# Kernel tuning notes

Hardware: AMD Instinct MI355X
Metric: run time of the kernel (lower is better)

The kernel has to match this reference:

```python
import jax, jax.numpy as jnp
import numpy as np

B, N, S, P, D = 128, 4096, 32, 64, 128  # batch, wafers, stages, PMs, embed dim
NORM = 300.0


def gather(src, idx):
    # src: [B, n, D], idx: [B, m] int -> [B, m, D]
    return jnp.take_along_axis(src, idx[:, :, None], axis=1)


def setup_inputs() -> dict:
    key = jax.random.key(0)
    ks = jax.random.split(key, 16)
    return {
        "encoded_row": jax.random.normal(ks[0], (B, N, D), jnp.float32),
        "encoded_col": jax.random.normal(ks[1], (B, S, D), jnp.float32),
        "clock": jax.random.uniform(ks[2], (B, 1), jnp.float32) * NORM,
        "loc_process_end_time": jax.random.uniform(ks[3], (B, P), jnp.float32) * (2.0 * NORM),
        "W_dyn": jax.random.normal(ks[4], (2, D), jnp.float32) * 0.05,
        "W_concat": jax.random.normal(ks[5], (3 * D, D), jnp.float32) * 0.05,
        "W_robot": jax.random.normal(ks[6], (3 * D, D), jnp.float32) * 0.05,
        "loc_hold_wafer": jax.random.randint(ks[7], (B, P), 0, N),
        "loc_stage": jax.random.randint(ks[8], (B, P), 1, S + 1),
        "robot_arm1_loc": jax.random.randint(ks[9], (B, 1), 0, P + 2),
        "robot_arm2_loc": jax.random.randint(ks[10], (B, 1), 0, P + 2),
        "arm1_recipe": jax.random.randint(ks[11], (B, 1), 0, N),
        "arm2_recipe": jax.random.randint(ks[12], (B, 1), 0, N),
        "arm1_next_stage": jax.random.randint(ks[13], (B, 1), 0, S + 2),
        "arm2_next_stage": jax.random.randint(ks[14], (B, 1), 0, S + 2),
    }


def reference(encoded_row, encoded_col, clock, loc_process_end_time,
              W_dyn, W_concat, W_robot,
              loc_hold_wafer, loc_stage, robot_arm1_loc, robot_arm2_loc,
              arm1_recipe, arm2_recipe, arm1_next_stage, arm2_next_stage):
    dt = encoded_row.dtype
    # ---- get_PM_embedding ----
    clk = jnp.broadcast_to(clock, (B, P))
    remain_prs = jnp.where(loc_process_end_time > clk,
                           loc_process_end_time - clk, 0.0) / NORM
    remain_purge = jnp.zeros_like(remain_prs)
    pm_dyn = jnp.stack([remain_prs, remain_purge], axis=-1) @ W_dyn  # [B,P,D]

    rows_dummy = jnp.concatenate(
        [encoded_row, jnp.zeros((B, 1, D), dt)], axis=1)          # [B,N+1,D]
    lot_idx = jnp.where(loc_hold_wafer >= 0, loc_hold_wafer, N)
    pm_wafer = gather(rows_dummy, lot_idx)                         # [B,P,D]
    pm_stage = gather(encoded_col, loc_stage - 1)                  # [B,P,D]
    pm_emb = jnp.concatenate([pm_stage, pm_wafer, pm_dyn], -1) @ W_concat

    # ---- get_robot_embedding ----
    loc_emb = jnp.concatenate(
        [jnp.zeros((B, 1, D), dt), pm_emb, jnp.ones((B, 1, D), dt)], axis=1)
    cols_pad = jnp.concatenate(
        [jnp.zeros((B, 1, D), dt), encoded_col, jnp.zeros((B, 1, D), dt)], axis=1)

    def arm_embed(loc_idx, recipe, next_stage):
        a_loc = gather(loc_emb, loc_idx)                           # [B,1,D]
        a_wafer = gather(rows_dummy, jnp.where(recipe >= 0, recipe, N))
        a_ns = gather(cols_pad, jnp.where(next_stage >= 0, next_stage, 0))
        return jnp.concatenate([a_loc, a_wafer, a_ns], -1) @ W_robot

    arm1 = arm_embed(robot_arm1_loc, arm1_recipe, arm1_next_stage)
    arm2 = arm_embed(robot_arm2_loc, arm2_recipe, arm2_next_stage)

    return jnp.concatenate([pm_emb, arm1, arm2], axis=1)           # [B,P+2,D]
```

## Files before the change

kernel.cpp:

```cpp
#include <hip/hip_runtime.h>
#include <stdint.h>

namespace {
constexpr int B = 128;
constexpr int N = 4096;
constexpr int S = 32;
constexpr int P = 64;
constexpr int D = 128;
constexpr int K = 384;
constexpr int KS = K / 32;
constexpr int ROWPAD = 196;
}

typedef __attribute__((ext_vector_type(8))) short short8;
typedef __attribute__((ext_vector_type(4))) float f32x4;

__device__ __forceinline__ uint32_t f2bf(float f) {
    union { float f; uint32_t u; } v; v.f = f;
    return (v.u + 0x7FFFu + ((v.u >> 16) & 1u)) >> 16;
}
__device__ __forceinline__ uint32_t pack2(float x, float y) {
    return f2bf(x) | (f2bf(y) << 16);
}
__device__ __forceinline__ float blo(uint32_t u) {
    union { uint32_t u; float f; } t; t.u = u << 16; return t.f;
}
__device__ __forceinline__ float bhi(uint32_t u) {
    union { uint32_t u; float f; } t; t.u = u & 0xFFFF0000u; return t.f;
}

__global__ __launch_bounds__(256) void prep_w_kernel(
    const float* __restrict__ W, uint32_t* __restrict__ Wsw)
{
    const int idx = blockIdx.x * 256 + threadIdx.x;
    const int n  = idx & 15;
    const int t  = (idx >> 4) & 7;
    const int q  = (idx >> 7) & 3;
    const int ks = idx >> 9;
    const int col  = t * 16 + n;
    const int krow = ks * 32 + q * 8;
    uint32_t pk[4];
    #pragma unroll
    for (int jj = 0; jj < 4; ++jj) {
        const float a = W[(size_t)(krow + 2 * jj) * D + col];
        const float b = W[(size_t)(krow + 2 * jj + 1) * D + col];
        pk[jj] = pack2(a, b);
    }
    ((uint4*)Wsw)[idx] = make_uint4(pk[0], pk[1], pk[2], pk[3]);
}

__global__ __launch_bounds__(256) void pm_gemm_kernel(
    const float* __restrict__ enc_row,
    const float* __restrict__ enc_col,
    const float* __restrict__ clockp,
    const float* __restrict__ lpet,
    const float* __restrict__ W_dyn,
    const int*   __restrict__ lhw,
    const int*   __restrict__ lstage,
    const uint32_t* __restrict__ Wsw,
    float* __restrict__ out)
{
    __shared__ uint32_t xs[16 * ROWPAD];
    const int lane = threadIdx.x & 63;
    const int wave = threadIdx.x >> 6;
    const int r0 = blockIdx.x * 16;

    const float2 wd = ((const float2*)W_dyn)[lane];
    #pragma unroll
    for (int rr = 0; rr < 4; ++rr) {
        const int r = wave * 4 + rr;
        const int rid = r0 + r;
        const int b = rid >> 6;
        const float c = clockp[b];
        const float tt = lpet[rid];
        const float rem = (tt > c) ? (tt - c) * (1.0f / 300.0f) : 0.0f;
        const int wi = lhw[rid];
        const int cs = lstage[rid] - 1;

        const float2 sv = ((const float2*)(enc_col + ((size_t)b * S + cs) * D))[lane];
        float2 wv = make_float2(0.f, 0.f);
        if (wi >= 0)
            wv = ((const float2*)(enc_row + ((size_t)b * N + wi) * D))[lane];

        xs[r * ROWPAD + 0 * 64 + lane] = pack2(sv.x, sv.y);
        xs[r * ROWPAD + 1 * 64 + lane] = pack2(wv.x, wv.y);
        xs[r * ROWPAD + 2 * 64 + lane] = pack2(wd.x * rem, wd.y * rem);
    }
    __syncthreads();

    const int q = lane >> 4;
    const int n16 = lane & 15;
    const int t0 = wave * 2, t1 = t0 + 1;

    f32x4 acc0 = {0.f, 0.f, 0.f, 0.f};
    f32x4 acc1 = {0.f, 0.f, 0.f, 0.f};
    const short8* wsw = (const short8*)Wsw;

    #pragma unroll
    for (int ks = 0; ks < KS; ++ks) {
        const short8 a = *(const short8*)(xs + n16 * ROWPAD + ks * 16 + q * 4);
        const short8 b0 = wsw[((ks * 4 + q) * 8 + t0) * 16 + n16];
        const short8 b1 = wsw[((ks * 4 + q) * 8 + t1) * 16 + n16];
        acc0 = __builtin_amdgcn_mfma_f32_16x16x32_bf16(a, b0, acc0, 0, 0, 0);
        acc1 = __builtin_amdgcn_mfma_f32_16x16x32_bf16(a, b1, acc1, 0, 0, 0);
    }

    #pragma unroll
    for (int i = 0; i < 4; ++i) {
        const int row = q * 4 + i;
        const int rid = r0 + row;
        const int bb = rid >> 6;
        const int pp = rid & 63;
        float* o = out + ((size_t)bb * (P + 2) + pp) * D;
        o[t0 * 16 + n16] = acc0[i];
        o[t1 * 16 + n16] = acc1[i];
    }
}

__global__ __launch_bounds__(64) void arm_kernel(
    const float* __restrict__ enc_row,
    const float* __restrict__ enc_col,
    const float* __restrict__ W_robot,
    const int* __restrict__ loc1, const int* __restrict__ loc2,
    const int* __restrict__ rec1, const int* __restrict__ rec2,
    const int* __restrict__ nst1, const int* __restrict__ nst2,
    float* __restrict__ out)
{
    __shared__ uint32_t xs[K / 2];
    const int lane = threadIdx.x;
    const int b = blockIdx.x >> 1;
    const int arm = blockIdx.x & 1;
    const int loc = arm ? loc2[b] : loc1[b];
    const int rec = arm ? rec2[b] : rec1[b];
    int ns = arm ? nst2[b] : nst1[b];
    if (ns < 0) ns = 0;

    float2 lv = make_float2(0.f, 0.f);
    if (loc >= 1 && loc <= P)
        lv = ((const float2*)(out + ((size_t)b * (P + 2) + (loc - 1)) * D))[lane];
    else if (loc == P + 1)
        lv = make_float2(1.f, 1.f);
    float2 wv = make_float2(0.f, 0.f);
    if (rec >= 0)
        wv = ((const float2*)(enc_row + ((size_t)b * N + rec) * D))[lane];
    float2 nv = make_float2(0.f, 0.f);
    if (ns >= 1 && ns <= S)
        nv = ((const float2*)(enc_col + ((size_t)b * S + (ns - 1)) * D))[lane];

    xs[0 * 64 + lane] = pack2(lv.x, lv.y);
    xs[1 * 64 + lane] = pack2(wv.x, wv.y);
    xs[2 * 64 + lane] = pack2(nv.x, nv.y);
    __syncthreads();

    float acc0 = 0.f, acc1 = 0.f;
    for (int kc = 0; kc < K / 8; ++kc) {
        const uint4 xq = *(const uint4*)&xs[kc * 4];
        float xv[8];
        xv[0] = blo(xq.x); xv[1] = bhi(xq.x);
        xv[2] = blo(xq.y); xv[3] = bhi(xq.y);
        xv[4] = blo(xq.z); xv[5] = bhi(xq.z);
        xv[6] = blo(xq.w); xv[7] = bhi(xq.w);
        #pragma unroll
        for (int kk = 0; kk < 8; ++kk) {
            const float w0 = W_robot[(kc * 8 + kk) * D + lane];
            const float w1 = W_robot[(kc * 8 + kk) * D + lane + 64];
            acc0 = fmaf(xv[kk], w0, acc0);
            acc1 = fmaf(xv[kk], w1, acc1);
        }
    }
    const size_t o = ((size_t)b * (P + 2) + P + arm) * D + lane;
    out[o] = acc0;
    out[o + 64] = acc1;
}

extern "C" void kernel_launch(void* const* d_in, const int* in_sizes, int n_in,
                              void* d_out, int out_size, void* d_ws, size_t ws_size,
                              hipStream_t stream) {
    const float* enc_row  = (const float*)d_in[0];
    const float* enc_col  = (const float*)d_in[1];
    const float* clockp   = (const float*)d_in[2];
    const float* lpet     = (const float*)d_in[3];
    const float* W_dyn    = (const float*)d_in[4];
    const float* W_concat = (const float*)d_in[5];
    const float* W_robot  = (const float*)d_in[6];
    const int*   lhw      = (const int*)d_in[7];
    const int*   lstage   = (const int*)d_in[8];
    const int*   loc1     = (const int*)d_in[9];
    const int*   loc2     = (const int*)d_in[10];
    const int*   rec1     = (const int*)d_in[11];
    const int*   rec2     = (const int*)d_in[12];
    const int*   nst1     = (const int*)d_in[13];
    const int*   nst2     = (const int*)d_in[14];
    float* out = (float*)d_out;
    uint32_t* Wsw = (uint32_t*)d_ws;

    prep_w_kernel<<<24, 256, 0, stream>>>(W_concat, Wsw);
    pm_gemm_kernel<<<(B * P) / 16, 256, 0, stream>>>(
        enc_row, enc_col, clockp, lpet, W_dyn, lhw, lstage, Wsw, out);
    arm_kernel<<<2 * B, 64, 0, stream>>>(
        enc_row, enc_col, W_robot, loc1, loc2, rec1, rec2, nst1, nst2, out);
}
```

Before: 340.5 us.

## Fuse arm embedding into PM GEMM kernel with MFMA and recomputed PM rows

Removes the separate arm kernel. Extra blocks in the PM GEMM launch recompute the needed PM embedding rows themselves, so they no longer wait on the PM output, then run the robot projection with bf16 MFMA using a pre-swizzled W_robot prepared alongside W_concat. This drops one kernel launch and the serial dependency between the two GEMMs, and replaces the scalar fp32 FMA loop. The cost is redundant PM row computation and extra bf16 rounding of the intermediate PM embedding before the second GEMM.

```diff
diff --git a/kernel.cpp b/kernel.cpp
--- a/kernel.cpp
+++ b/kernel.cpp
@@ -10,6 +10,8 @@
 constexpr int K = 384;
 constexpr int KS = K / 32;
 constexpr int ROWPAD = 196;
+constexpr int PM_BLOCKS = (B * P) / 16;
+constexpr int ARM_BLOCKS = (2 * B) / 16;
 }
 
 typedef __attribute__((ext_vector_type(8))) short short8;
@@ -22,21 +24,19 @@
 __device__ __forceinline__ uint32_t pack2(float x, float y) {
     return f2bf(x) | (f2bf(y) << 16);
 }
-__device__ __forceinline__ float blo(uint32_t u) {
-    union { uint32_t u; float f; } t; t.u = u << 16; return t.f;
-}
-__device__ __forceinline__ float bhi(uint32_t u) {
-    union { uint32_t u; float f; } t; t.u = u & 0xFFFF0000u; return t.f;
-}
 
 __global__ __launch_bounds__(256) void prep_w_kernel(
-    const float* __restrict__ W, uint32_t* __restrict__ Wsw)
+    const float* __restrict__ Wc, const float* __restrict__ Wr,
+    uint32_t* __restrict__ Wsw)
 {
     const int idx = blockIdx.x * 256 + threadIdx.x;
-    const int n  = idx & 15;
-    const int t  = (idx >> 4) & 7;
-    const int q  = (idx >> 7) & 3;
-    const int ks = idx >> 9;
+    const bool is_c = (idx < 6144);
+    const float* W = is_c ? Wc : Wr;
+    const int l = is_c ? idx : (idx - 6144);
+    const int n  = l & 15;
+    const int t  = (l >> 4) & 7;
+    const int q  = (l >> 7) & 3;
+    const int ks = l >> 9;
     const int col  = t * 16 + n;
     const int krow = ks * 32 + q * 8;
     uint32_t pk[4];
@@ -49,7 +49,7 @@
     ((uint4*)Wsw)[idx] = make_uint4(pk[0], pk[1], pk[2], pk[3]);
 }
 
-__global__ __launch_bounds__(256) void pm_gemm_kernel(
+__global__ __launch_bounds__(256) void fused_kernel(
     const float* __restrict__ enc_row,
     const float* __restrict__ enc_col,
     const float* __restrict__ clockp,
@@ -57,120 +57,157 @@
     const float* __restrict__ W_dyn,
     const int*   __restrict__ lhw,
     const int*   __restrict__ lstage,
+    const int* __restrict__ loc1, const int* __restrict__ loc2,
+    const int* __restrict__ rec1, const int* __restrict__ rec2,
+    const int* __restrict__ nst1, const int* __restrict__ nst2,
     const uint32_t* __restrict__ Wsw,
     float* __restrict__ out)
 {
     __shared__ uint32_t xs[16 * ROWPAD];
+    __shared__ uint32_t xs2[16 * ROWPAD];
+    __shared__ int locs[16];
+
     const int lane = threadIdx.x & 63;
     const int wave = threadIdx.x >> 6;
-    const int r0 = blockIdx.x * 16;
-
-    const float2 wd = ((const float2*)W_dyn)[lane];
-    #pragma unroll
-    for (int rr = 0; rr < 4; ++rr) {
-        const int r = wave * 4 + rr;
-        const int rid = r0 + r;
-        const int b = rid >> 6;
-        const float c = clockp[b];
-        const float tt = lpet[rid];
-        const float rem = (tt > c) ? (tt - c) * (1.0f / 300.0f) : 0.0f;
-        const int wi = lhw[rid];
-        const int cs = lstage[rid] - 1;
-
-        const float2 sv = ((const float2*)(enc_col + ((size_t)b * S + cs) * D))[lane];
-        float2 wv = make_float2(0.f, 0.f);
-        if (wi >= 0)
-            wv = ((const float2*)(enc_row + ((size_t)b * N + wi) * D))[lane];
-
-        xs[r * ROWPAD + 0 * 64 + lane] = pack2(sv.x, sv.y);
-        xs[r * ROWPAD + 1 * 64 + lane] = pack2(wv.x, wv.y);
-        xs[r * ROWPAD + 2 * 64 + lane] = pack2(wd.x * rem, wd.y * rem);
-    }
-    __syncthreads();
-
     const int q = lane >> 4;
     const int n16 = lane & 15;
     const int t0 = wave * 2, t1 = t0 + 1;
-
-    f32x4 acc0 = {0.f, 0.f, 0.f, 0.f};
-    f32x4 acc1 = {0.f, 0.f, 0.f, 0.f};
-    const short8* wsw = (const short8*)Wsw;
-
-    #pragma unroll
-    for (int ks = 0; ks < KS; ++ks) {
-        const short8 a = *(const short8*)(xs + n16 * ROWPAD + ks * 16 + q * 4);
-        const short8 b0 = wsw[((ks * 4 + q) * 8 + t0) * 16 + n16];
-        const short8 b1 = wsw[((ks * 4 + q) * 8 + t1) * 16 + n16];
-        acc0 = __builtin_amdgcn_mfma_f32_16x16x32_bf16(a, b0, acc0, 0, 0, 0);
-        acc1 = __builtin_amdgcn_mfma_f32_16x16x32_bf16(a, b1, acc1, 0, 0, 0);
+    const short8* wswc = (const short8*)Wsw;
+    const short8* wswr = wswc + 6144;
+    const float2 wd = ((const float2*)W_dyn)[lane];
+
+    if (blockIdx.x < PM_BLOCKS) {
+        const int r0 = blockIdx.x * 16;
+        #pragma unroll
+        for (int rr = 0; rr < 4; ++rr) {
+            const int r = wave * 4 + rr;
+            const int rid = r0 + r;
+            const int b = rid >> 6;
+            const float c = clockp[b];
+            const float tt = lpet[rid];
+            const float rem = (tt > c) ? (tt - c) * (1.0f / 300.0f) : 0.0f;
+            const int wi = lhw[rid];
+            const int cs = lstage[rid] - 1;
+            const float2 sv = ((const float2*)(enc_col + ((size_t)b * S + cs) * D))[lane];
+            float2 wv = make_float2(0.f, 0.f);
+            if (wi >= 0)
+                wv = ((const float2*)(enc_row + ((size_t)b * N + wi) * D))[lane];
+            xs[r * ROWPAD + 0 * 64 + lane] = pack2(sv.x, sv.y);
+            xs[r * ROWPAD + 1 * 64 + lane] = pack2(wv.x, wv.y);
+            xs[r * ROWPAD + 2 * 64 + lane] = pack2(wd.x * rem, wd.y * rem);
+        }
+        __syncthreads();
+
+        f32x4 acc0 = {0.f, 0.f, 0.f, 0.f};
+        f32x4 acc1 = {0.f, 0.f, 0.f, 0.f};
+        #pragma unroll
+        for (int ks = 0; ks < KS; ++ks) {
+            const short8 a = *(const short8*)(xs + n16 * ROWPAD + ks * 16 + q * 4);
+            const short8 b0 = wswc[((ks * 4 + q) * 8 + t0) * 16 + n16];
+            const short8 b1 = wswc[((ks * 4 + q) * 8 + t1) * 16 + n16];
+            acc0 = __builtin_amdgcn_mfma_f32_16x16x32_bf16(a, b0, acc0, 0, 0, 0);
+            acc1 = __builtin_amdgcn_mfma_f32_16x16x32_bf16(a, b1, acc1, 0, 0, 0);
+        }
+        #pragma unroll
+        for (int i = 0; i < 4; ++i) {
+            const int row = q * 4 + i;
+            const int rid = r0 + row;
+            const int bb = rid >> 6;
+            const int pp = rid & 63;
+            float* o = out + ((size_t)bb * (P + 2) + pp) * D;
+            o[t0 * 16 + n16] = acc0[i];
+            o[t1 * 16 + n16] = acc1[i];
+        }
+    } else {
+        const int ab = blockIdx.x - PM_BLOCKS;
+        #pragma unroll
+        for (int rr = 0; rr < 4; ++rr) {
+            const int r = wave * 4 + rr;
+            const int aid = ab * 16 + r;
+            const int b = aid >> 1;
+            const int arm = aid & 1;
+            const int loc = arm ? loc2[b] : loc1[b];
+            const int rec = arm ? rec2[b] : rec1[b];
+            int ns = arm ? nst2[b] : nst1[b];
+            if (ns < 0) ns = 0;
+            if (lane == 0) locs[r] = loc;
+
+            if (loc >= 1 && loc <= P) {
+                const int rid = b * P + (loc - 1);
+                const float c = clockp[b];
+                const float tt = lpet[rid];
+                const float rem = (tt > c) ? (tt - c) * (1.0f / 300.0f) : 0.0f;
+                const int wi = lhw[rid];
+                const int cs = lstage[rid] - 1;
+                const float2 sv = ((const float2*)(enc_col + ((size_t)b * S + cs) * D))[lane];
+                float2 wv = make_float2(0.f, 0.f);
+                if (wi >= 0)
+                    wv = ((const float2*)(enc_row + ((size_t)b * N + wi) * D))[lane];
+                xs[r * ROWPAD + 0 * 64 + lane] = pack2(sv.x, sv.y);
+                xs[r * ROWPAD + 1 * 64 + lane] = pack2(wv.x, wv.y);
+                xs[r * ROWPAD + 2 * 64 + lane] = pack2(wd.x * rem, wd.y * rem);
+            } else {
+                xs[r * ROWPAD + 0 * 64 + lane] = 0u;
+                xs[r * ROWPAD + 1 * 64 + lane] = 0u;
+                xs[r * ROWPAD + 2 * 64 + lane] = 0u;
+            }
+
+            float2 awv = make_float2(0.f, 0.f);
+            if (rec >= 0)
+                awv = ((const float2*)(enc_row + ((size_t)b * N + rec) * D))[lane];
+            float2 anv = make_float2(0.f, 0.f);
+            if (ns >= 1 && ns <= S)
+                anv = ((const float2*)(enc_col + ((size_t)b * S + (ns - 1)) * D))[lane];
+            xs2[r * ROWPAD + 1 * 64 + lane] = pack2(awv.x, awv.y);
+            xs2[r * ROWPAD + 2 * 64 + lane] = pack2(anv.x, anv.y);
+        }
+        __syncthreads();
+
+        f32x4 acc0 = {0.f, 0.f, 0.f, 0.f};
+        f32x4 acc1 = {0.f, 0.f, 0.f, 0.f};
+        #pragma unroll
+        for (int ks = 0; ks < KS; ++ks) {
+            const short8 a = *(const short8*)(xs + n16 * ROWPAD + ks * 16 + q * 4);
+            const short8 b0 = wswc[((ks * 4 + q) * 8 + t0) * 16 + n16];
+            const short8 b1 = wswc[((ks * 4 + q) * 8 + t1) * 16 + n16];
+            acc0 = __builtin_amdgcn_mfma_f32_16x16x32_bf16(a, b0, acc0, 0, 0, 0);
+            acc1 = __builtin_amdgcn_mfma_f32_16x16x32_bf16(a, b1, acc1, 0, 0, 0);
+        }
+
+        unsigned short* u2 = (unsigned short*)xs2;
+        #pragma unroll
+        for (int i = 0; i < 4; ++i) {
+            const int row = q * 4 + i;
+            const int lc = locs[row];
+            float v0 = acc0[i], v1 = acc1[i];
+            if (lc == 0)      { v0 = 0.f; v1 = 0.f; }
+            if (lc == P + 1)  { v0 = 1.f; v1 = 1.f; }
+            u2[row * (2 * ROWPAD) + t0 * 16 + n16] = (unsigned short)f2bf(v0);
+            u2[row * (2 * ROWPAD) + t1 * 16 + n16] = (unsigned short)f2bf(v1);
+        }
+        __syncthreads();
+
+        f32x4 racc0 = {0.f, 0.f, 0.f, 0.f};
+        f32x4 racc1 = {0.f, 0.f, 0.f, 0.f};
+        #pragma unroll
+        for (int ks = 0; ks < KS; ++ks) {
+            const short8 a = *(const short8*)(xs2 + n16 * ROWPAD + ks * 16 + q * 4);
+            const short8 b0 = wswr[((ks * 4 + q) * 8 + t0) * 16 + n16];
+            const short8 b1 = wswr[((ks * 4 + q) * 8 + t1) * 16 + n16];
+            racc0 = __builtin_amdgcn_mfma_f32_16x16x32_bf16(a, b0, racc0, 0, 0, 0);
+            racc1 = __builtin_amdgcn_mfma_f32_16x16x32_bf16(a, b1, racc1, 0, 0, 0);
+        }
+        #pragma unroll
+        for (int i = 0; i < 4; ++i) {
+            const int row = q * 4 + i;
+            const int aid = ab * 16 + row;
+            const int bb = aid >> 1;
+            const int arm = aid & 1;
+            float* o = out + ((size_t)bb * (P + 2) + P + arm) * D;
+            o[t0 * 16 + n16] = racc0[i];
+            o[t1 * 16 + n16] = racc1[i];
+        }
     }
-
-    #pragma unroll
-    for (int i = 0; i < 4; ++i) {
-        const int row = q * 4 + i;
-        const int rid = r0 + row;
-        const int bb = rid >> 6;
-        const int pp = rid & 63;
-        float* o = out + ((size_t)bb * (P + 2) + pp) * D;
-        o[t0 * 16 + n16] = acc0[i];
-        o[t1 * 16 + n16] = acc1[i];
-    }
-}
-
-__global__ __launch_bounds__(64) void arm_kernel(
-    const float* __restrict__ enc_row,
-    const float* __restrict__ enc_col,
-    const float* __restrict__ W_robot,
-    const int* __restrict__ loc1, const int* __restrict__ loc2,
-    const int* __restrict__ rec1, const int* __restrict__ rec2,
-    const int* __restrict__ nst1, const int* __restrict__ nst2,
-    float* __restrict__ out)
-{
-    __shared__ uint32_t xs[K / 2];
-    const int lane = threadIdx.x;
-    const int b = blockIdx.x >> 1;
-    const int arm = blockIdx.x & 1;
-    const int loc = arm ? loc2[b] : loc1[b];
-    const int rec = arm ? rec2[b] : rec1[b];
-    int ns = arm ? nst2[b] : nst1[b];
-    if (ns < 0) ns = 0;
-
-    float2 lv = make_float2(0.f, 0.f);
-    if (loc >= 1 && loc <= P)
-        lv = ((const float2*)(out + ((size_t)b * (P + 2) + (loc - 1)) * D))[lane];
-    else if (loc == P + 1)
-        lv = make_float2(1.f, 1.f);
-    float2 wv = make_float2(0.f, 0.f);
-    if (rec >= 0)
-        wv = ((const float2*)(enc_row + ((size_t)b * N + rec) * D))[lane];
-    float2 nv = make_float2(0.f, 0.f);
-    if (ns >= 1 && ns <= S)
-        nv = ((const float2*)(enc_col + ((size_t)b * S + (ns - 1)) * D))[lane];
-
-    xs[0 * 64 + lane] = pack2(lv.x, lv.y);
-    xs[1 * 64 + lane] = pack2(wv.x, wv.y);
-    xs[2 * 64 + lane] = pack2(nv.x, nv.y);
-    __syncthreads();
-
-    float acc0 = 0.f, acc1 = 0.f;
-    for (int kc = 0; kc < K / 8; ++kc) {
-        const uint4 xq = *(const uint4*)&xs[kc * 4];
-        float xv[8];
-        xv[0] = blo(xq.x); xv[1] = bhi(xq.x);
-        xv[2] = blo(xq.y); xv[3] = bhi(xq.y);
-        xv[4] = blo(xq.z); xv[5] = bhi(xq.z);
-        xv[6] = blo(xq.w); xv[7] = bhi(xq.w);
-        #pragma unroll
-        for (int kk = 0; kk < 8; ++kk) {
-            const float w0 = W_robot[(kc * 8 + kk) * D + lane];
-            const float w1 = W_robot[(kc * 8 + kk) * D + lane + 64];
-            acc0 = fmaf(xv[kk], w0, acc0);
-            acc1 = fmaf(xv[kk], w1, acc1);
-        }
-    }
-    const size_t o = ((size_t)b * (P + 2) + P + arm) * D + lane;
-    out[o] = acc0;
-    out[o + 64] = acc1;
 }
 
 extern "C" void kernel_launch(void* const* d_in, const int* in_sizes, int n_in,
@@ -194,9 +231,8 @@
     float* out = (float*)d_out;
     uint32_t* Wsw = (uint32_t*)d_ws;
 
-    prep_w_kernel<<<24, 256, 0, stream>>>(W_concat, Wsw);
-    pm_gemm_kernel<<<(B * P) / 16, 256, 0, stream>>>(
-        enc_row, enc_col, clockp, lpet, W_dyn, lhw, lstage, Wsw, out);
-    arm_kernel<<<2 * B, 64, 0, stream>>>(
-        enc_row, enc_col, W_robot, loc1, loc2, rec1, rec2, nst1, nst2, out);
-}
+    prep_w_kernel<<<48, 256, 0, stream>>>(W_concat, W_robot, Wsw);
+    fused_kernel<<<PM_BLOCKS + ARM_BLOCKS, 256, 0, stream>>>(
+        enc_row, enc_col, clockp, lpet, W_dyn, lhw, lstage,
+        loc1, loc2, rec1, rec2, nst1, nst2, Wsw, out);
+}
```

Result: faster. 330.4 us (-3.0%).
